# Optimization experiments

Hardware: AMD Instinct MI355X
Metric: run time of the kernel (lower is better)

Reference implementation:

```python
import jax, jax.numpy as jnp
import numpy as np
from jax import lax

D = 64
EPS = 1e-8


def zc_rmsnorm(x, g):
    x0 = x - jnp.mean(x, axis=-1, keepdims=True)
    return x0 * jax.lax.rsqrt(jnp.mean(x0 * x0, axis=-1, keepdims=True) + EPS) * g


def l2norm(x):
    return x * jax.lax.rsqrt(jnp.sum(x * x, axis=-1, keepdims=True) + EPS)


def linear(x, w, b):
    # w: [out, in] (torch layout), x: [..., in]
    return jnp.einsum('btd,od->bto', x, w) + b


def dwconv3(x, w, b):
    # x: [B, T, D]; w: [D, 1, 3] depthwise kernel; padding=1 (SAME)
    xT = jnp.transpose(x, (0, 2, 1))  # [B, D, T]
    y = lax.conv_general_dilated(
        xT, w, window_strides=(1,), padding=[(1, 1)],
        dimension_numbers=('NCH', 'OIH', 'NCH'), feature_group_count=D)
    y = y + b[None, :, None]
    return jnp.transpose(y, (0, 2, 1))  # [B, T, D]


def setup_inputs() -> dict:
    key = jax.random.key(0)
    ks = jax.random.split(key, 24)
    s = 1.0 / np.sqrt(D)
    def lin_wb(k1, k2):
        return (jax.random.uniform(k1, (D, D), jnp.float32, -s, s),
                jax.random.uniform(k2, (D,), jnp.float32, -s, s))
    def conv_wb(k1, k2):
        cs = 1.0 / np.sqrt(3.0)
        return (jax.random.uniform(k1, (D, 1, 3), jnp.float32, -cs, cs),
                jax.random.uniform(k2, (D,), jnp.float32, -cs, cs))
    x = jax.random.normal(ks[0], (64, 4096, D), jnp.float32)
    qw, qb = lin_wb(ks[1], ks[2]); kw, kb = lin_wb(ks[3], ks[4]); vw, vb = lin_wb(ks[5], ks[6])
    qcw, qcb = conv_wb(ks[7], ks[8]); kcw, kcb = conv_wb(ks[9], ks[10]); vcw, vcb = conv_wb(ks[11], ks[12])
    aw, ab = lin_wb(ks[13], ks[14]); bw, bb = lin_wb(ks[15], ks[16])
    pw, pb = lin_wb(ks[17], ks[18])
    return dict(x=x, norm_g=jnp.ones((D,), jnp.float32),
                qw=qw, qb=qb, kw=kw, kb=kb, vw=vw, vb=vb,
                qcw=qcw, qcb=qcb, kcw=kcw, kcb=kcb, vcw=vcw, vcb=vcb,
                aw=aw, ab=ab, bw=bw, bb=bb,
                post_norm_g=jnp.ones((D,), jnp.float32), pw=pw, pb=pb)


def reference(x, norm_g, qw, qb, kw, kb, vw, vb, qcw, qcb, kcw, kcb, vcw, vcb,
              aw, ab, bw, bb, post_norm_g, pw, pb):
    h = zc_rmsnorm(x, norm_g)
    q = jax.nn.sigmoid(dwconv3(linear(h, qw, qb), qcw, qcb))
    k = jax.nn.sigmoid(dwconv3(linear(h, kw, kb), kcw, kcb))
    v = jax.nn.sigmoid(dwconv3(linear(h, vw, vb), vcw, vcb))
    q, k = l2norm(q), l2norm(k)
    delta = q * (k * v)
    delta = jnp.tanh(linear(x, aw, ab)) * delta + linear(x, bw, bb)
    dhat = linear(zc_rmsnorm(delta, post_norm_g), pw, pb)
    # dropout in eval mode (identity)
    return x + jax.nn.sigmoid(jax.nn.silu(dhat)) * dhat
```

## Files before the change

kernel.cpp:

```cpp
#include <hip/hip_runtime.h>


#define TBS 32
#define ROWS 34
#define DD 64
#define T_LEN 4096
#define TILES_PB 128
#define LSTRIDE 72

typedef unsigned short ushort_t;
typedef short bf16x8 __attribute__((ext_vector_type(8)));
typedef float f32x4 __attribute__((ext_vector_type(4)));
typedef float f32x16 __attribute__((ext_vector_type(16)));

__device__ inline float lo2f(unsigned u) { return __uint_as_float(u << 16); }
__device__ inline float hi2f(unsigned u) { return __uint_as_float(u & 0xffff0000u); }
__device__ inline unsigned pk2(float a, float b) {
    unsigned r;
    asm("v_cvt_pk_bf16_f32 %0, %1, %2" : "=v"(r) : "v"(a), "v"(b));
    return r;
}
__device__ inline ushort_t f2b(float f) {
    unsigned u = __float_as_uint(f);
    u += 0x7fffu + ((u >> 16) & 1u);
    return (ushort_t)(u >> 16);
}

__device__ inline float rcp_(float x) {
#if __has_builtin(__builtin_amdgcn_rcpf)
    return __builtin_amdgcn_rcpf(x);
#else
    float r; asm("v_rcp_f32 %0, %1" : "=v"(r) : "v"(x)); return r;
#endif
}
__device__ inline float rsq_(float x) {
#if __has_builtin(__builtin_amdgcn_rsqf)
    return __builtin_amdgcn_rsqf(x);
#else
    float r; asm("v_rsq_f32 %0, %1" : "=v"(r) : "v"(x)); return r;
#endif
}

template<int CTRL>
__device__ inline float dpp_add(float v) {
    int t = __builtin_amdgcn_mov_dpp(__float_as_int(v), CTRL, 0xf, 0xf, true);
    return v + __int_as_float(t);
}
__device__ inline float sum16(float v) {
    v = dpp_add<0x128>(v);
    v = dpp_add<0x124>(v);
    v = dpp_add<0x122>(v);
    v = dpp_add<0x121>(v);
    return v;
}

__device__ inline float sigmoidf_(float x) { return rcp_(1.f + __expf(-x)); }
__device__ inline float tanhf_(float x) {
    float xc = fminf(fmaxf(x, -15.f), 15.f);
    float e2 = __expf(2.f * xc);
    return (e2 - 1.f) * rcp_(e2 + 1.f);
}

__global__ __launch_bounds__(256) void cvt_kernel(
    const float* __restrict__ w0, const float* __restrict__ w1,
    const float* __restrict__ w2, const float* __restrict__ w3,
    const float* __restrict__ w4, const float* __restrict__ w5,
    ushort_t* __restrict__ dst) {
    int i = blockIdx.x * 256 + threadIdx.x;
    const float* ws_[6] = {w0, w1, w2, w3, w4, w5};
    dst[i] = f2b(ws_[i >> 12][i & 4095]);
}

__device__ inline void mm32(const ushort_t* __restrict__ W,
                            const float* __restrict__ bias,
                            const ushort_t* src, ushort_t* dst,
                            int m0, int strip, int lane) {
    const int l31  = lane & 31;
    const int half = lane >> 5;
    const int t    = m0 + l31;
    const ushort_t* wrow = W + (strip * 32 + l31) * 64 + half * 8;
    const ushort_t* arow = src + t * LSTRIDE + half * 8;
    f32x16 acc = {};
#pragma unroll
    for (int kk = 0; kk < 4; kk++) {
        bf16x8 af = *(const bf16x8*)(wrow + kk * 16);
        bf16x8 bf = *(const bf16x8*)(arow + kk * 16);
        acc = __builtin_amdgcn_mfma_f32_32x32x16_bf16(af, bf, acc, 0, 0, 0);
    }
#pragma unroll
    for (int rg = 0; rg < 4; rg++) {
        const int o0 = strip * 32 + rg * 8 + half * 4;
        f32x4 bv = *(const f32x4*)(bias + o0);
        uint2 w;
        w.x = pk2(acc[rg * 4 + 0] + bv[0], acc[rg * 4 + 1] + bv[1]);
        w.y = pk2(acc[rg * 4 + 2] + bv[2], acc[rg * 4 + 3] + bv[3]);
        *(uint2*)(dst + t * LSTRIDE + o0) = w;
    }
}

__device__ inline void conv_sig4(const float* __restrict__ CW,
                                 const float* __restrict__ CB, int cb,
                                 const ushort_t* F, int rr, bool zl, bool zr,
                                 float out[4]) {
    uint2 m_ = *(const uint2*)(F + (rr - 1) * LSTRIDE + cb);
    uint2 c_ = *(const uint2*)(F + rr * LSTRIDE + cb);
    uint2 p_ = *(const uint2*)(F + (rr + 1) * LSTRIDE + cb);
    f32x4 w0 = *(const f32x4*)(CW + cb);
    f32x4 w1 = *(const f32x4*)(CW + 64 + cb);
    f32x4 w2 = *(const f32x4*)(CW + 128 + cb);
    f32x4 bb = *(const f32x4*)(CB + cb);
    float xm[4] = {lo2f(m_.x), hi2f(m_.x), lo2f(m_.y), hi2f(m_.y)};
    float x0[4] = {lo2f(c_.x), hi2f(c_.x), lo2f(c_.y), hi2f(c_.y)};
    float xp[4] = {lo2f(p_.x), hi2f(p_.x), lo2f(p_.y), hi2f(p_.y)};
#pragma unroll
    for (int i = 0; i < 4; i++) {
        float a = fmaf(w0[i], zl ? 0.f : xm[i],
                  fmaf(w1[i], x0[i],
                  fmaf(w2[i], zr ? 0.f : xp[i], bb[i])));
        out[i] = sigmoidf_(a);
    }
}

__global__ __launch_bounds__(512, 8) void gdn_kernel(
    const float* __restrict__ xg, const float* __restrict__ norm_g,
    const ushort_t* __restrict__ wpack,
    const float* __restrict__ qcw, const float* __restrict__ qcb,
    const float* __restrict__ kcw, const float* __restrict__ kcb,
    const float* __restrict__ vcw, const float* __restrict__ vcb,
    const float* __restrict__ qbf, const float* __restrict__ kbf,
    const float* __restrict__ vbf, const float* __restrict__ abf,
    const float* __restrict__ bbf, const float* __restrict__ pbf,
    const float* __restrict__ post_g,
    float* __restrict__ outg, int tiles_per_b) {
    __shared__ __align__(16) ushort_t Xs[ROWS * LSTRIDE];
    __shared__ __align__(16) ushort_t Hs[ROWS * LSTRIDE];
    __shared__ __align__(16) ushort_t Fq[ROWS * LSTRIDE];
    __shared__ __align__(16) ushort_t Fk[ROWS * LSTRIDE];
    __shared__ __align__(16) ushort_t Fv[ROWS * LSTRIDE];
    __shared__ __align__(16) ushort_t Fa[ROWS * LSTRIDE];
    __shared__ __align__(16) ushort_t Fb[ROWS * LSTRIDE];
    __shared__ __align__(16) float CWs[768];

    const int tid    = threadIdx.x;
    const int wave   = tid >> 6;
    const int lane   = tid & 63;
    const int cb     = (tid & 15) * 4;
    const int rgrp   = tid >> 4;
    const int bidx = blockIdx.x;
    const int b    = bidx >> 7;
    const int tile = bidx & (TILES_PB - 1);
    const int t0   = tile * TBS;
    const bool left_edge  = (t0 == 0);
    const bool right_edge = (t0 + TBS >= T_LEN);

    {
        const f32x4 gv = *(const f32x4*)(norm_g + cb);
        for (int r = rgrp; r < ROWS; r += 32) {
            int t = t0 + r - 1;
            f32x4 xv = {0.f, 0.f, 0.f, 0.f};
            if (t >= 0 && t < T_LEN)
                xv = *(const f32x4*)(xg + ((size_t)b * T_LEN + t) * DD + cb);
            float s  = (xv[0] + xv[1]) + (xv[2] + xv[3]);
            float s2 = 0.f;
#pragma unroll
            for (int i = 0; i < 4; i++) s2 = fmaf(xv[i], xv[i], s2);
            s = sum16(s); s2 = sum16(s2);
            float mean = s * (1.f / 64.f);
            float var  = fmaxf(fmaf(-mean, mean, s2 * (1.f / 64.f)), 0.f);
            float inv  = rsq_(var + 1e-8f);
            uint2 xpk; xpk.x = pk2(xv[0], xv[1]); xpk.y = pk2(xv[2], xv[3]);
            *(uint2*)(Xs + r * LSTRIDE + cb) = xpk;
            uint2 hpk;
            hpk.x = pk2((xv[0] - mean) * inv * gv[0], (xv[1] - mean) * inv * gv[1]);
            hpk.y = pk2((xv[2] - mean) * inv * gv[2], (xv[3] - mean) * inv * gv[3]);
            *(uint2*)(Hs + r * LSTRIDE + cb) = hpk;
        }
    }
    if (tid < 192) {
        int tap = tid >> 6, c = tid & 63;
        CWs[tid]       = qcw[c * 3 + tap];
        CWs[192 + tid] = kcw[c * 3 + tap];
        CWs[384 + tid] = vcw[c * 3 + tap];
    } else if (tid < 256) {
        int c = tid - 192;
        CWs[576 + c] = qcb[c];
        CWs[640 + c] = kcb[c];
        CWs[704 + c] = vcb[c];
    }
    __syncthreads();

#pragma unroll
    for (int i = 0; i < 2; i++) {
        const int u = wave * 2 + i;
        const ushort_t* W; const float* bias; const ushort_t* src; ushort_t* dst;
        int m0, strip;
        if (u < 12) {
            const int g = u >> 2, sub = u & 3;
            W = wpack + g * 4096;
            bias = (g == 0) ? qbf : (g == 1) ? kbf : vbf;
            dst  = (g == 0) ? Fq  : (g == 1) ? Fk  : Fv;
            src = Hs;
            m0 = (sub & 2) ? 2 : 0;
            strip = sub & 1;
        } else {
            const int g = (u - 12) >> 1;
            W = wpack + (3 + g) * 4096;
            bias = g ? bbf : abf;
            dst  = g ? Fb  : Fa;
            src = Xs;
            m0 = 1;
            strip = u & 1;
        }
        mm32(W, bias, src, dst, m0, strip, lane);
    }
    __syncthreads();

    {
        const int rr = rgrp + 1;
        const bool zl = (rr == 1) && left_edge;
        const bool zr = (rr == TBS) && right_edge;
        float qs[4], ks[4], vs[4];
        conv_sig4(CWs,       CWs + 576, cb, Fq, rr, zl, zr, qs);
        conv_sig4(CWs + 192, CWs + 640, cb, Fk, rr, zl, zr, ks);
        conv_sig4(CWs + 384, CWs + 704, cb, Fv, rr, zl, zr, vs);
        float sq = 0.f, sk = 0.f;
#pragma unroll
        for (int i = 0; i < 4; i++) {
            sq = fmaf(qs[i], qs[i], sq);
            sk = fmaf(ks[i], ks[i], sk);
        }
        float qi = rsq_(sum16(sq) + 1e-8f);
        float ki = rsq_(sum16(sk) + 1e-8f);
        uint2 av = *(const uint2*)(Fa + rr * LSTRIDE + cb);
        uint2 bv = *(const uint2*)(Fb + rr * LSTRIDE + cb);
        float af[4] = {lo2f(av.x), hi2f(av.x), lo2f(av.y), hi2f(av.y)};
        float bf[4] = {lo2f(bv.x), hi2f(bv.x), lo2f(bv.y), hi2f(bv.y)};
        float d2[4]; float sm = 0.f, sm2 = 0.f;
#pragma unroll
        for (int i = 0; i < 4; i++) {
            float delta = (qs[i] * qi) * (ks[i] * ki) * vs[i];
            d2[i] = fmaf(tanhf_(af[i]), delta, bf[i]);
            sm += d2[i];
            sm2 = fmaf(d2[i], d2[i], sm2);
        }
        sm = sum16(sm); sm2 = sum16(sm2);
        float mean = sm * (1.f / 64.f);
        float var  = fmaxf(fmaf(-mean, mean, sm2 * (1.f / 64.f)), 0.f);
        float inv  = rsq_(var + 1e-8f);
        const f32x4 pgv = *(const f32x4*)(post_g + cb);
        uint2 npk;
        npk.x = pk2((d2[0] - mean) * inv * pgv[0], (d2[1] - mean) * inv * pgv[1]);
        npk.y = pk2((d2[2] - mean) * inv * pgv[2], (d2[3] - mean) * inv * pgv[3]);
        *(uint2*)(Hs + rr * LSTRIDE + cb) = npk;
    }
    __syncthreads();

    if (wave < 2)
        mm32(wpack + 5 * 4096, pbf, Hs, Fq, 1, wave, lane);
    __syncthreads();

    {
        const int rr = rgrp + 1;
        const int t = t0 + rgrp;
        uint2 dpk = *(const uint2*)(Fq + rr * LSTRIDE + cb);
        float dh[4] = {lo2f(dpk.x), hi2f(dpk.x), lo2f(dpk.y), hi2f(dpk.y)};
        const float* xrow = xg + ((size_t)b * T_LEN + t) * DD + cb;
        f32x4 xv = *(const f32x4*)(xrow);
        f32x4 ov;
#pragma unroll
        for (int i = 0; i < 4; i++) {
            float sl = dh[i] * sigmoidf_(dh[i]);
            ov[i] = xv[i] + sigmoidf_(sl) * dh[i];
        }
        *(f32x4*)(outg + ((size_t)b * T_LEN + t) * DD + cb) = ov;
    }
}

extern "C" void kernel_launch(void* const* d_in, const int* in_sizes, int n_in,
                              void* d_out, int out_size, void* d_ws, size_t ws_size,
                              hipStream_t stream) {
    const float* xg     = (const float*)d_in[0];
    const float* norm_g = (const float*)d_in[1];
    const float* qw  = (const float*)d_in[2];
    const float* qb  = (const float*)d_in[3];
    const float* kw  = (const float*)d_in[4];
    const float* kb  = (const float*)d_in[5];
    const float* vw  = (const float*)d_in[6];
    const float* vb  = (const float*)d_in[7];
    const float* qcw = (const float*)d_in[8];
    const float* qcb = (const float*)d_in[9];
    const float* kcw = (const float*)d_in[10];
    const float* kcb = (const float*)d_in[11];
    const float* vcw = (const float*)d_in[12];
    const float* vcb = (const float*)d_in[13];
    const float* aw  = (const float*)d_in[14];
    const float* ab  = (const float*)d_in[15];
    const float* bw  = (const float*)d_in[16];
    const float* bb  = (const float*)d_in[17];
    const float* pg  = (const float*)d_in[18];
    const float* pw  = (const float*)d_in[19];
    const float* pb  = (const float*)d_in[20];

    ushort_t* wpack = (ushort_t*)d_ws;

    hipLaunchKernelGGL(cvt_kernel, dim3(96), dim3(256), 0, stream,
                       qw, kw, vw, aw, bw, pw, wpack);

    const int B = in_sizes[0] / (T_LEN * DD);
    const int tiles_per_b = T_LEN / TBS;
    hipLaunchKernelGGL(gdn_kernel, dim3(B * tiles_per_b), dim3(512), 0, stream,
                       xg, norm_g, wpack, qcw, qcb, kcw, kcb, vcw, vcb,
                       qb, kb, vb, ab, bb, pb, pg,
                       (float*)d_out, tiles_per_b);
}
```

Measured before the change: 234.9 us.

## Enlarge time tile to 128 rows with 1024-thread blocks

```diff
diff --git a/kernel.cpp b/kernel.cpp
--- a/kernel.cpp
+++ b/kernel.cpp
@@ -1,11 +1,11 @@
 #include <hip/hip_runtime.h>
 
 
-#define TBS 32
-#define ROWS 34
+#define TBS 128
+#define ROWS 130
 #define DD 64
 #define T_LEN 4096
-#define TILES_PB 128
+#define TILES_PB 32
 #define LSTRIDE 72
 
 typedef unsigned short ushort_t;
@@ -121,7 +121,7 @@
     }
 }
 
-__global__ __launch_bounds__(512, 8) void gdn_kernel(
+__global__ __launch_bounds__(1024, 4) void gdn_kernel(
     const float* __restrict__ xg, const float* __restrict__ norm_g,
     const ushort_t* __restrict__ wpack,
     const float* __restrict__ qcw, const float* __restrict__ qcb,
@@ -131,7 +131,7 @@
     const float* __restrict__ vbf, const float* __restrict__ abf,
     const float* __restrict__ bbf, const float* __restrict__ pbf,
     const float* __restrict__ post_g,
-    float* __restrict__ outg, int tiles_per_b) {
+    float* __restrict__ outg) {
     __shared__ __align__(16) ushort_t Xs[ROWS * LSTRIDE];
     __shared__ __align__(16) ushort_t Hs[ROWS * LSTRIDE];
     __shared__ __align__(16) ushort_t Fq[ROWS * LSTRIDE];
@@ -147,7 +147,7 @@
     const int cb     = (tid & 15) * 4;
     const int rgrp   = tid >> 4;
     const int bidx = blockIdx.x;
-    const int b    = bidx >> 7;
+    const int b    = bidx >> 5;
     const int tile = bidx & (TILES_PB - 1);
     const int t0   = tile * TBS;
     const bool left_edge  = (t0 == 0);
@@ -155,7 +155,7 @@
 
     {
         const f32x4 gv = *(const f32x4*)(norm_g + cb);
-        for (int r = rgrp; r < ROWS; r += 32) {
+        auto do_row = [&](int r) {
             int t = t0 + r - 1;
             f32x4 xv = {0.f, 0.f, 0.f, 0.f};
             if (t >= 0 && t < T_LEN)
@@ -174,7 +174,10 @@
             hpk.x = pk2((xv[0] - mean) * inv * gv[0], (xv[1] - mean) * inv * gv[1]);
             hpk.y = pk2((xv[2] - mean) * inv * gv[2], (xv[3] - mean) * inv * gv[3]);
             *(uint2*)(Hs + r * LSTRIDE + cb) = hpk;
-        }
+        };
+        do_row(rgrp);
+        do_row(rgrp + 64);
+        if (rgrp == 16 || rgrp == 17) do_row(rgrp + 112);
     }
     if (tid < 192) {
         int tap = tid >> 6, c = tid & 63;
@@ -189,34 +192,39 @@
     }
     __syncthreads();
 
-#pragma unroll
-    for (int i = 0; i < 2; i++) {
-        const int u = wave * 2 + i;
-        const ushort_t* W; const float* bias; const ushort_t* src; ushort_t* dst;
-        int m0, strip;
-        if (u < 12) {
-            const int g = u >> 2, sub = u & 3;
-            W = wpack + g * 4096;
-            bias = (g == 0) ? qbf : (g == 1) ? kbf : vbf;
-            dst  = (g == 0) ? Fq  : (g == 1) ? Fk  : Fv;
-            src = Hs;
-            m0 = (sub & 2) ? 2 : 0;
-            strip = sub & 1;
-        } else {
-            const int g = (u - 12) >> 1;
-            W = wpack + (3 + g) * 4096;
-            bias = g ? bbf : abf;
-            dst  = g ? Fb  : Fa;
-            src = Xs;
-            m0 = 1;
-            strip = u & 1;
+    {
+        const int m0tab[5] = {0, 32, 64, 96, 98};
+#pragma unroll
+        for (int i = 0; i < 3; i++) {
+            const int u = wave + 16 * i;
+            if (u >= 46) break;
+            const ushort_t* W; const float* bias; const ushort_t* src; ushort_t* dst;
+            int m0, strip;
+            if (u < 30) {
+                const int g = u / 10, r = u % 10;
+                W = wpack + g * 4096;
+                bias = (g == 0) ? qbf : (g == 1) ? kbf : vbf;
+                dst  = (g == 0) ? Fq  : (g == 1) ? Fk  : Fv;
+                src = Hs;
+                strip = r & 1;
+                m0 = m0tab[r >> 1];
+            } else {
+                const int j = u - 30, g = j >> 3, r = j & 7;
+                W = wpack + (3 + g) * 4096;
+                bias = g ? bbf : abf;
+                dst  = g ? Fb  : Fa;
+                src = Xs;
+                strip = r & 1;
+                m0 = 1 + 32 * (r >> 1);
+            }
+            mm32(W, bias, src, dst, m0, strip, lane);
         }
-        mm32(W, bias, src, dst, m0, strip, lane);
     }
     __syncthreads();
 
-    {
-        const int rr = rgrp + 1;
+#pragma unroll
+    for (int half_t = 0; half_t < 2; half_t++) {
+        const int rr = rgrp + 1 + half_t * 64;
         const bool zl = (rr == 1) && left_edge;
         const bool zr = (rr == TBS) && right_edge;
         float qs[4], ks[4], vs[4];
@@ -255,14 +263,15 @@
     }
     __syncthreads();
 
-    if (wave < 2)
-        mm32(wpack + 5 * 4096, pbf, Hs, Fq, 1, wave, lane);
+    if (wave < 8)
+        mm32(wpack + 5 * 4096, pbf, Hs, Fq, 1 + 32 * (wave >> 1), wave & 1, lane);
     __syncthreads();
 
-    {
-        const int rr = rgrp + 1;
-        const int t = t0 + rgrp;
-        uint2 dpk = *(const uint2*)(Fq + rr * LSTRIDE + cb);
+#pragma unroll
+    for (int half_t = 0; half_t < 2; half_t++) {
+        const int tr = rgrp + half_t * 64;
+        const int t  = t0 + tr;
+        uint2 dpk = *(const uint2*)(Fq + (tr + 1) * LSTRIDE + cb);
         float dh[4] = {lo2f(dpk.x), hi2f(dpk.x), lo2f(dpk.y), hi2f(dpk.y)};
         const float* xrow = xg + ((size_t)b * T_LEN + t) * DD + cb;
         f32x4 xv = *(const f32x4*)(xrow);
@@ -307,9 +316,8 @@
                        qw, kw, vw, aw, bw, pw, wpack);
 
     const int B = in_sizes[0] / (T_LEN * DD);
-    const int tiles_per_b = T_LEN / TBS;
-    hipLaunchKernelGGL(gdn_kernel, dim3(B * tiles_per_b), dim3(512), 0, stream,
+    hipLaunchKernelGGL(gdn_kernel, dim3(B * TILES_PB), dim3(1024), 0, stream,
                        xg, norm_g, wpack, qcw, qcb, kcw, kcb, vcw, vcb,
                        qb, kb, vb, ab, bb, pb, pg,
-                       (float*)d_out, tiles_per_b);
-}
+                       (float*)d_out);
+}
```

Result: slower. 248.0 us (+5.6%).
